# Optimization experiments

Measured on AMD Instinct MI355X. Metric: run time of the kernel, lower is better.

## Reference

```python
import jax, jax.numpy as jnp
import numpy as np

NUM_EXPERTS = 8
IN_F = 1024
OUT_F = 1024
N_TOK = 8192


def setup_inputs() -> dict:
    key = jax.random.key(0)
    ks = jax.random.split(key, 5)
    scale_in = 1.0 / np.sqrt(IN_F)
    x = jax.random.normal(ks[0], (N_TOK, IN_F), dtype=jnp.float32)
    # stacked expert weights [E, in, out] and biases [E, out]
    We = jax.random.uniform(ks[1], (NUM_EXPERTS, IN_F, OUT_F), dtype=jnp.float32, minval=-scale_in, maxval=scale_in)
    be = jax.random.uniform(ks[2], (NUM_EXPERTS, OUT_F), dtype=jnp.float32, minval=-scale_in, maxval=scale_in)
    # gate: Linear(in_features, num_experts)
    Wg = jax.random.uniform(ks[3], (IN_F, NUM_EXPERTS), dtype=jnp.float32, minval=-scale_in, maxval=scale_in)
    bg = jax.random.uniform(ks[4], (NUM_EXPERTS,), dtype=jnp.float32, minval=-scale_in, maxval=scale_in)
    return {"x": x, "We": We, "be": be, "Wg": Wg, "bg": bg}


def reference(x, We, be, Wg, bg):
    # gate_score: softmax over experts  [N, E]
    gate_score = jax.nn.softmax(x @ Wg + bg, axis=-1)
    # all-experts dense outputs  [N, E, out]
    expert_outputs = jnp.einsum('ni,eio->neo', x, We) + be[None, :, :]
    # gate-weighted combine  [N, out]
    return jnp.einsum('ne,neo->no', gate_score, expert_outputs)
```

## Files before the change

### kernel.cpp

```cpp
#include <hip/hip_runtime.h>
#include <hip/hip_bf16.h>

#define M_TOK 8192
#define IN_F  1024
#define OUT_F 1024
#define N_EXP 8
#define KT    8192

typedef __attribute__((ext_vector_type(8))) _Float16 f16x8;
typedef __attribute__((ext_vector_type(4))) _Float16 f16x4;
typedef __attribute__((ext_vector_type(4))) float    f32x4;

__global__ void moe_prep_kernel(const float* __restrict__ x, const float* __restrict__ Wg,
                                const float* __restrict__ bg, const float* __restrict__ We,
                                float* __restrict__ g, _Float16* __restrict__ xh,
                                _Float16* __restrict__ wt) {
    __shared__ float t[64][65];
    if (blockIdx.x < 2048) {
        int token = blockIdx.x * 4 + (threadIdx.x >> 6);
        int lane  = threadIdx.x & 63;
        const float* xr = x + (size_t)token * IN_F;
        float4 xv[4];
        float acc[8] = {0.f,0.f,0.f,0.f,0.f,0.f,0.f,0.f};
#pragma unroll
        for (int kc = 0; kc < 4; ++kc) {
            int i = kc * 256 + lane * 4;
            xv[kc] = *(const float4*)(xr + i);
            float xj[4] = {xv[kc].x, xv[kc].y, xv[kc].z, xv[kc].w};
#pragma unroll
            for (int j = 0; j < 4; ++j) {
                const float4* wr = (const float4*)(Wg + (size_t)(i + j) * 8);
                float4 w0 = wr[0], w1 = wr[1];
                acc[0] = fmaf(xj[j], w0.x, acc[0]); acc[1] = fmaf(xj[j], w0.y, acc[1]);
                acc[2] = fmaf(xj[j], w0.z, acc[2]); acc[3] = fmaf(xj[j], w0.w, acc[3]);
                acc[4] = fmaf(xj[j], w1.x, acc[4]); acc[5] = fmaf(xj[j], w1.y, acc[5]);
                acc[6] = fmaf(xj[j], w1.z, acc[6]); acc[7] = fmaf(xj[j], w1.w, acc[7]);
            }
        }
#pragma unroll
        for (int e = 0; e < 8; ++e) {
            float v = acc[e];
#pragma unroll
            for (int off = 32; off > 0; off >>= 1) v += __shfl_xor(v, off, 64);
            acc[e] = v + bg[e];
        }
        float mx = acc[0];
#pragma unroll
        for (int e = 1; e < 8; ++e) mx = fmaxf(mx, acc[e]);
        float sum = 0.f;
#pragma unroll
        for (int e = 0; e < 8; ++e) { acc[e] = __expf(acc[e] - mx); sum += acc[e]; }
        float inv = 1.0f / sum;
#pragma unroll
        for (int e = 0; e < 8; ++e) acc[e] *= inv;
        if (lane == 0) {
            float4 p0 = {acc[0], acc[1], acc[2], acc[3]};
            float4 p1 = {acc[4], acc[5], acc[6], acc[7]};
            float4* gp = (float4*)(g + (size_t)token * 8);
            gp[0] = p0; gp[1] = p1;
        }
        _Float16* xhr = xh + (size_t)token * IN_F;
#pragma unroll
        for (int kc = 0; kc < 4; ++kc) {
            f16x4 h = { (_Float16)xv[kc].x, (_Float16)xv[kc].y,
                        (_Float16)xv[kc].z, (_Float16)xv[kc].w };
            *(f16x4*)(xhr + kc * 256 + lane * 4) = h;
        }
    } else {
        int bid = blockIdx.x - 2048;
        int e  = bid >> 8;
        int o0 = ((bid >> 4) & 15) * 64;
        int i0 = (bid & 15) * 64;
        const float* src = We + ((size_t)e << 20);
        int oo = threadIdx.x & 63;
        int ib = threadIdx.x >> 6;
#pragma unroll
        for (int r = 0; r < 16; ++r) {
            int i = ib + r * 4;
            t[i][oo] = src[(size_t)(i0 + i) * OUT_F + o0 + oo];
        }
        __syncthreads();
#pragma unroll
        for (int r = 0; r < 16; ++r) {
            int o = ib + r * 4;
            wt[(size_t)(o0 + o) * KT + (size_t)e * 1024 + i0 + oo] = (_Float16)t[oo][o];
        }
    }
}

__device__ __forceinline__ void async16(const void* gp, void* lp) {
    __builtin_amdgcn_global_load_lds((const __attribute__((address_space(1))) void*)gp,
                                     (__attribute__((address_space(3))) void*)lp, 16, 0, 0);
}

__global__ __launch_bounds__(256, 2) void moe_gemm_kernel(
    const _Float16* __restrict__ xh,
    const _Float16* __restrict__ wt,
    const float* __restrict__ g,
    const float* __restrict__ be,
    float* __restrict__ out)
{
    __shared__ __align__(16) _Float16 As[128 * 64];
    __shared__ __align__(16) _Float16 Bs[128 * 64];
    __shared__ float gs[8 * 128];
    __shared__ float bs[8 * 128];

    const int tid  = threadIdx.x;
    const int lane = tid & 63;
    const int wave = tid >> 6;
    const size_t n0 = (size_t)blockIdx.x * 128;
    const size_t m0 = (size_t)blockIdx.y * 128;

    {
        float4 v = ((const float4*)(g + m0 * 8))[tid];
        int row = tid >> 1, e0 = (tid & 1) * 4;
        gs[(e0 + 0) * 128 + row] = v.x;
        gs[(e0 + 1) * 128 + row] = v.y;
        gs[(e0 + 2) * 128 + row] = v.z;
        gs[(e0 + 3) * 128 + row] = v.w;
    }
#pragma unroll
    for (int r = 0; r < 4; ++r) {
        int idx = r * 256 + tid;
        int eb = idx >> 7, col = idx & 127;
        bs[idx] = be[(size_t)eb * 1024 + n0 + col];
    }
    __syncthreads();

    const int rb = tid >> 3;
    const int c8 = (tid & 7) ^ (rb & 7);
    const _Float16* pA = xh + (m0 + rb) * (size_t)IN_F + c8 * 8;
    const _Float16* pB = wt + (n0 + rb) * (size_t)KT + c8 * 8;
    char* lA = (char*)As + tid * 16;
    char* lB = (char*)Bs + tid * 16;

    const int quad = lane >> 4;
    const int ml   = lane & 15;
    const int wm   = (wave >> 1) * 64;
    const int wn   = (wave & 1) * 64;
    const int raA0 = (wm + ml) * 128 + (((0 * 4 + quad) ^ (lane & 7)) * 16);
    const int raA1 = (wm + ml) * 128 + (((1 * 4 + quad) ^ (lane & 7)) * 16);
    const int raB0 = (wn + ml) * 128 + (((0 * 4 + quad) ^ (lane & 7)) * 16);
    const int raB1 = (wn + ml) * 128 + (((1 * 4 + quad) ^ (lane & 7)) * 16);

    f32x4 acc[4][4] = {};
#pragma unroll
    for (int e = 0; e < 8; ++e) {
        float ge[4][4], bb[4];
#pragma unroll
        for (int i = 0; i < 4; ++i)
#pragma unroll
            for (int r = 0; r < 4; ++r) ge[i][r] = gs[e * 128 + wm + i * 16 + quad * 4 + r];
#pragma unroll
        for (int jn = 0; jn < 4; ++jn) bb[jn] = bs[e * 128 + wn + jn * 16 + ml];
#pragma unroll
        for (int i = 0; i < 4; ++i)
#pragma unroll
            for (int jn = 0; jn < 4; ++jn)
#pragma unroll
                for (int r = 0; r < 4; ++r)
                    acc[i][jn][r] = fmaf(ge[i][r], bb[jn], acc[i][jn][r]);
    }

    _Float16 gh[8][4];
#pragma unroll
    for (int e = 0; e < 8; ++e)
#pragma unroll
        for (int t = 0; t < 4; ++t)
            gh[e][t] = (_Float16)gs[e * 128 + wm + t * 16 + ml];

    for (int kt = 0; kt < 16; ++kt) {
        const _Float16* sA = pA + kt * 64;
#pragma unroll
        for (int j = 0; j < 4; ++j) async16(sA + j * 32 * (size_t)IN_F, lA + j * 4096);

        f16x8 afr[2][4];
#pragma unroll
        for (int e = 0; e < 8; ++e) {
            const _Float16* sB = pB + e * 1024 + kt * 64;
#pragma unroll
            for (int j = 0; j < 4; ++j) async16(sB + j * 32 * (size_t)KT, lB + j * 4096);
            __syncthreads();
            if (e == 0) {
#pragma unroll
                for (int t = 0; t < 4; ++t) {
                    afr[0][t] = *(const f16x8*)((const char*)As + raA0 + t * 2048);
                    afr[1][t] = *(const f16x8*)((const char*)As + raA1 + t * 2048);
                }
            }
#pragma unroll
            for (int s = 0; s < 2; ++s) {
                const int rB = s ? raB1 : raB0;
                f16x8 af[4], bf[4];
#pragma unroll
                for (int t = 0; t < 4; ++t) bf[t] = *(const f16x8*)((const char*)Bs + rB + t * 2048);
#pragma unroll
                for (int t = 0; t < 4; ++t) af[t] = afr[s][t] * gh[e][t];
#pragma unroll
                for (int i = 0; i < 4; ++i)
#pragma unroll
                    for (int jn = 0; jn < 4; ++jn)
                        acc[i][jn] = __builtin_amdgcn_mfma_f32_16x16x32_f16(af[i], bf[jn], acc[i][jn], 0, 0, 0);
            }
            __syncthreads();
        }
    }

#pragma unroll
    for (int i = 0; i < 4; ++i) {
        const int rowb = wm + i * 16 + quad * 4;
#pragma unroll
        for (int jn = 0; jn < 4; ++jn) {
            const size_t col = n0 + wn + jn * 16 + ml;
#pragma unroll
            for (int r = 0; r < 4; ++r)
                out[(m0 + rowb + r) * (size_t)OUT_F + col] = acc[i][jn][r];
        }
    }
}

extern "C" void kernel_launch(void* const* d_in, const int* in_sizes, int n_in,
                              void* d_out, int out_size, void* d_ws, size_t ws_size,
                              hipStream_t stream) {
    const float* x  = (const float*)d_in[0];
    const float* We = (const float*)d_in[1];
    const float* be = (const float*)d_in[2];
    const float* Wg = (const float*)d_in[3];
    const float* bg = (const float*)d_in[4];
    float* out = (float*)d_out;

    char* ws = (char*)d_ws;
    float*    g   = (float*)ws;
    _Float16* xh  = (_Float16*)(ws + (1 << 18));
    _Float16* wt2 = (_Float16*)(ws + (1 << 18) + (1 << 24));

    moe_prep_kernel<<<4096, 256, 0, stream>>>(x, Wg, bg, We, g, xh, wt2);
    moe_gemm_kernel<<<dim3(OUT_F / 128, M_TOK / 128), 256, 0, stream>>>(xh, wt2, g, be, out);
}
```

Measured before the change: 253.7 us.

## Double-buffer B tiles with async prefetch and split prep into gate/transpose kernels

The GEMM loop now prefetches the next expert's B tile, or the next k-step's A and B tiles, into a second LDS buffer before waiting. Explicit vmcnt waits and raw barriers let the global-to-LDS loads overlap the MFMA work instead of stalling on every expert. The prep kernel is split in two: a gate kernel that handles four tokens per wave to reuse Wg loads, and a transpose kernel that writes 16-byte vectorized fp16 stores. The costs are an extra kernel launch, extra LDS for the second B buffer, and hand-written wait counts that must match the number of outstanding loads.

```diff
diff --git a/kernel.cpp b/kernel.cpp
--- a/kernel.cpp
+++ b/kernel.cpp
@@ -11,80 +11,100 @@
 typedef __attribute__((ext_vector_type(4))) _Float16 f16x4;
 typedef __attribute__((ext_vector_type(4))) float    f32x4;
 
-__global__ void moe_prep_kernel(const float* __restrict__ x, const float* __restrict__ Wg,
-                                const float* __restrict__ bg, const float* __restrict__ We,
-                                float* __restrict__ g, _Float16* __restrict__ xh,
-                                _Float16* __restrict__ wt) {
+__global__ __launch_bounds__(256) void moe_gate_kernel(
+    const float* __restrict__ x, const float* __restrict__ Wg,
+    const float* __restrict__ bg, float* __restrict__ g, _Float16* __restrict__ xh)
+{
+    const int lane = threadIdx.x & 63;
+    const int wave = threadIdx.x >> 6;
+    const int t0 = blockIdx.x * 16 + wave * 4;
+    const float* xr0 = x + (size_t)t0 * IN_F;
+
+    float acc[4][8] = {};
+#pragma unroll
+    for (int kc = 0; kc < 4; ++kc) {
+        const int i = kc * 256 + lane * 4;
+        float4 xv[4];
+#pragma unroll
+        for (int tk = 0; tk < 4; ++tk) xv[tk] = *(const float4*)(xr0 + (size_t)tk * IN_F + i);
+        float xs[4][4];
+#pragma unroll
+        for (int tk = 0; tk < 4; ++tk) {
+            xs[tk][0] = xv[tk].x; xs[tk][1] = xv[tk].y;
+            xs[tk][2] = xv[tk].z; xs[tk][3] = xv[tk].w;
+        }
+#pragma unroll
+        for (int j = 0; j < 4; ++j) {
+            const float4* wr = (const float4*)(Wg + (size_t)(i + j) * 8);
+            float4 w0 = wr[0], w1 = wr[1];
+            float wv[8] = {w0.x, w0.y, w0.z, w0.w, w1.x, w1.y, w1.z, w1.w};
+#pragma unroll
+            for (int tk = 0; tk < 4; ++tk)
+#pragma unroll
+                for (int e = 0; e < 8; ++e)
+                    acc[tk][e] = fmaf(xs[tk][j], wv[e], acc[tk][e]);
+        }
+#pragma unroll
+        for (int tk = 0; tk < 4; ++tk) {
+            f16x4 h = { (_Float16)xs[tk][0], (_Float16)xs[tk][1],
+                        (_Float16)xs[tk][2], (_Float16)xs[tk][3] };
+            *(f16x4*)(xh + (size_t)(t0 + tk) * IN_F + i) = h;
+        }
+    }
+#pragma unroll
+    for (int tk = 0; tk < 4; ++tk) {
+        float a[8];
+#pragma unroll
+        for (int e = 0; e < 8; ++e) {
+            float v = acc[tk][e];
+#pragma unroll
+            for (int off = 32; off > 0; off >>= 1) v += __shfl_xor(v, off, 64);
+            a[e] = v + bg[e];
+        }
+        float mx = a[0];
+#pragma unroll
+        for (int e = 1; e < 8; ++e) mx = fmaxf(mx, a[e]);
+        float sum = 0.f;
+#pragma unroll
+        for (int e = 0; e < 8; ++e) { a[e] = __expf(a[e] - mx); sum += a[e]; }
+        float inv = 1.0f / sum;
+        if (lane == 0) {
+            float4 p0 = {a[0] * inv, a[1] * inv, a[2] * inv, a[3] * inv};
+            float4 p1 = {a[4] * inv, a[5] * inv, a[6] * inv, a[7] * inv};
+            float4* gp = (float4*)(g + (size_t)(t0 + tk) * 8);
+            gp[0] = p0; gp[1] = p1;
+        }
+    }
+}
+
+__global__ __launch_bounds__(256) void moe_transpose_kernel(
+    const float* __restrict__ We, _Float16* __restrict__ wt)
+{
     __shared__ float t[64][65];
-    if (blockIdx.x < 2048) {
-        int token = blockIdx.x * 4 + (threadIdx.x >> 6);
-        int lane  = threadIdx.x & 63;
-        const float* xr = x + (size_t)token * IN_F;
-        float4 xv[4];
-        float acc[8] = {0.f,0.f,0.f,0.f,0.f,0.f,0.f,0.f};
-#pragma unroll
-        for (int kc = 0; kc < 4; ++kc) {
-            int i = kc * 256 + lane * 4;
-            xv[kc] = *(const float4*)(xr + i);
-            float xj[4] = {xv[kc].x, xv[kc].y, xv[kc].z, xv[kc].w};
-#pragma unroll
-            for (int j = 0; j < 4; ++j) {
-                const float4* wr = (const float4*)(Wg + (size_t)(i + j) * 8);
-                float4 w0 = wr[0], w1 = wr[1];
-                acc[0] = fmaf(xj[j], w0.x, acc[0]); acc[1] = fmaf(xj[j], w0.y, acc[1]);
-                acc[2] = fmaf(xj[j], w0.z, acc[2]); acc[3] = fmaf(xj[j], w0.w, acc[3]);
-                acc[4] = fmaf(xj[j], w1.x, acc[4]); acc[5] = fmaf(xj[j], w1.y, acc[5]);
-                acc[6] = fmaf(xj[j], w1.z, acc[6]); acc[7] = fmaf(xj[j], w1.w, acc[7]);
-            }
-        }
-#pragma unroll
-        for (int e = 0; e < 8; ++e) {
-            float v = acc[e];
-#pragma unroll
-            for (int off = 32; off > 0; off >>= 1) v += __shfl_xor(v, off, 64);
-            acc[e] = v + bg[e];
-        }
-        float mx = acc[0];
-#pragma unroll
-        for (int e = 1; e < 8; ++e) mx = fmaxf(mx, acc[e]);
-        float sum = 0.f;
-#pragma unroll
-        for (int e = 0; e < 8; ++e) { acc[e] = __expf(acc[e] - mx); sum += acc[e]; }
-        float inv = 1.0f / sum;
-#pragma unroll
-        for (int e = 0; e < 8; ++e) acc[e] *= inv;
-        if (lane == 0) {
-            float4 p0 = {acc[0], acc[1], acc[2], acc[3]};
-            float4 p1 = {acc[4], acc[5], acc[6], acc[7]};
-            float4* gp = (float4*)(g + (size_t)token * 8);
-            gp[0] = p0; gp[1] = p1;
-        }
-        _Float16* xhr = xh + (size_t)token * IN_F;
-#pragma unroll
-        for (int kc = 0; kc < 4; ++kc) {
-            f16x4 h = { (_Float16)xv[kc].x, (_Float16)xv[kc].y,
-                        (_Float16)xv[kc].z, (_Float16)xv[kc].w };
-            *(f16x4*)(xhr + kc * 256 + lane * 4) = h;
-        }
-    } else {
-        int bid = blockIdx.x - 2048;
-        int e  = bid >> 8;
-        int o0 = ((bid >> 4) & 15) * 64;
-        int i0 = (bid & 15) * 64;
-        const float* src = We + ((size_t)e << 20);
-        int oo = threadIdx.x & 63;
-        int ib = threadIdx.x >> 6;
-#pragma unroll
-        for (int r = 0; r < 16; ++r) {
-            int i = ib + r * 4;
-            t[i][oo] = src[(size_t)(i0 + i) * OUT_F + o0 + oo];
-        }
-        __syncthreads();
-#pragma unroll
-        for (int r = 0; r < 16; ++r) {
-            int o = ib + r * 4;
-            wt[(size_t)(o0 + o) * KT + (size_t)e * 1024 + i0 + oo] = (_Float16)t[oo][o];
-        }
+    const int bid = blockIdx.x;
+    const int e  = bid >> 8;
+    const int o0 = ((bid >> 4) & 15) * 64;
+    const int i0 = (bid & 15) * 64;
+    const float* src = We + ((size_t)e << 20);
+    const int oo = threadIdx.x & 63;
+    const int ib = threadIdx.x >> 6;
+#pragma unroll
+    for (int r = 0; r < 16; ++r) {
+        int i = ib + r * 4;
+        t[i][oo] = src[(size_t)(i0 + i) * OUT_F + o0 + oo];
+    }
+    __syncthreads();
+    const int i8 = threadIdx.x & 7;
+    const int ob = threadIdx.x >> 3;
+#pragma unroll
+    for (int h = 0; h < 2; ++h) {
+        const int o = ob + h * 32;
+        float v[8];
+#pragma unroll
+        for (int j = 0; j < 8; ++j) v[j] = t[i8 * 8 + j][o];
+        f16x8 hv = { (_Float16)v[0], (_Float16)v[1], (_Float16)v[2], (_Float16)v[3],
+                     (_Float16)v[4], (_Float16)v[5], (_Float16)v[6], (_Float16)v[7] };
+        *(f16x8*)(wt + (size_t)(o0 + o) * KT + (size_t)e * 1024 + i0 + i8 * 8) = hv;
     }
 }
 
@@ -101,7 +121,7 @@
     float* __restrict__ out)
 {
     __shared__ __align__(16) _Float16 As[128 * 64];
-    __shared__ __align__(16) _Float16 Bs[128 * 64];
+    __shared__ __align__(16) _Float16 Bs[2][128 * 64];
     __shared__ float gs[8 * 128];
     __shared__ float bs[8 * 128];
 
@@ -131,8 +151,9 @@
     const int c8 = (tid & 7) ^ (rb & 7);
     const _Float16* pA = xh + (m0 + rb) * (size_t)IN_F + c8 * 8;
     const _Float16* pB = wt + (n0 + rb) * (size_t)KT + c8 * 8;
-    char* lA = (char*)As + tid * 16;
-    char* lB = (char*)Bs + tid * 16;
+    char* lA  = (char*)As + tid * 16;
+    char* lB0 = (char*)Bs[0] + tid * 16;
+    char* lB1 = (char*)Bs[1] + tid * 16;
 
     const int quad = lane >> 4;
     const int ml   = lane & 15;
@@ -143,6 +164,11 @@
     const int raB0 = (wn + ml) * 128 + (((0 * 4 + quad) ^ (lane & 7)) * 16);
     const int raB1 = (wn + ml) * 128 + (((1 * 4 + quad) ^ (lane & 7)) * 16);
 
+#pragma unroll
+    for (int j = 0; j < 4; ++j) async16(pA + j * 32 * (size_t)IN_F, lA + j * 4096);
+#pragma unroll
+    for (int j = 0; j < 4; ++j) async16(pB + j * 32 * (size_t)KT, lB0 + j * 4096);
+
     f32x4 acc[4][4] = {};
 #pragma unroll
     for (int e = 0; e < 8; ++e) {
@@ -170,17 +196,30 @@
             gh[e][t] = (_Float16)gs[e * 128 + wm + t * 16 + ml];
 
     for (int kt = 0; kt < 16; ++kt) {
-        const _Float16* sA = pA + kt * 64;
-#pragma unroll
-        for (int j = 0; j < 4; ++j) async16(sA + j * 32 * (size_t)IN_F, lA + j * 4096);
-
         f16x8 afr[2][4];
 #pragma unroll
         for (int e = 0; e < 8; ++e) {
-            const _Float16* sB = pB + e * 1024 + kt * 64;
-#pragma unroll
-            for (int j = 0; j < 4; ++j) async16(sB + j * 32 * (size_t)KT, lB + j * 4096);
-            __syncthreads();
+            if (e < 7) {
+                const _Float16* sB = pB + (e + 1) * 1024 + kt * 64;
+                char* nB = ((e + 1) & 1) ? lB1 : lB0;
+#pragma unroll
+                for (int j = 0; j < 4; ++j) async16(sB + j * 32 * (size_t)KT, nB + j * 4096);
+                asm volatile("s_waitcnt vmcnt(4)" ::: "memory");
+            } else if (kt < 15) {
+                const _Float16* sA = pA + (kt + 1) * 64;
+#pragma unroll
+                for (int j = 0; j < 4; ++j) async16(sA + j * 32 * (size_t)IN_F, lA + j * 4096);
+                const _Float16* sB = pB + (kt + 1) * 64;
+#pragma unroll
+                for (int j = 0; j < 4; ++j) async16(sB + j * 32 * (size_t)KT, lB0 + j * 4096);
+                asm volatile("s_waitcnt vmcnt(8)" ::: "memory");
+            } else {
+                asm volatile("s_waitcnt vmcnt(0)" ::: "memory");
+            }
+            __builtin_amdgcn_s_barrier();
+            __builtin_amdgcn_sched_barrier(0);
+
+            const char* cB = (const char*)((e & 1) ? Bs[1] : Bs[0]);
             if (e == 0) {
 #pragma unroll
                 for (int t = 0; t < 4; ++t) {
@@ -193,7 +232,7 @@
                 const int rB = s ? raB1 : raB0;
                 f16x8 af[4], bf[4];
 #pragma unroll
-                for (int t = 0; t < 4; ++t) bf[t] = *(const f16x8*)((const char*)Bs + rB + t * 2048);
+                for (int t = 0; t < 4; ++t) bf[t] = *(const f16x8*)(cB + rB + t * 2048);
 #pragma unroll
                 for (int t = 0; t < 4; ++t) af[t] = afr[s][t] * gh[e][t];
 #pragma unroll
@@ -202,7 +241,9 @@
                     for (int jn = 0; jn < 4; ++jn)
                         acc[i][jn] = __builtin_amdgcn_mfma_f32_16x16x32_f16(af[i], bf[jn], acc[i][jn], 0, 0, 0);
             }
-            __syncthreads();
+            __builtin_amdgcn_sched_barrier(0);
+            __builtin_amdgcn_s_barrier();
+            __builtin_amdgcn_sched_barrier(0);
         }
     }
 
@@ -234,6 +275,7 @@
     _Float16* xh  = (_Float16*)(ws + (1 << 18));
     _Float16* wt2 = (_Float16*)(ws + (1 << 18) + (1 << 24));
 
-    moe_prep_kernel<<<4096, 256, 0, stream>>>(x, Wg, bg, We, g, xh, wt2);
+    moe_gate_kernel<<<512, 256, 0, stream>>>(x, Wg, bg, g, xh);
+    moe_transpose_kernel<<<2048, 256, 0, stream>>>(We, wt2);
     moe_gemm_kernel<<<dim3(OUT_F / 128, M_TOK / 128), 256, 0, stream>>>(xh, wt2, g, be, out);
 }
```

Result: slower. 324.3 us (+27.8%).
